# Performance work log

Hardware: AMD Instinct MI355X
Metric: run time of the kernel (lower is better)

## Reference

```python
import jax, jax.numpy as jnp
import numpy as np

N_NODES = 100000
N_EDGES = 3200000
D_FEAT = 256
HIDDEN = 16


def setup_inputs() -> dict:
    key = jax.random.key(0)
    k1, k2, k3, k4 = jax.random.split(key, 4)
    x = jax.random.normal(k1, (N_NODES, D_FEAT), dtype=jnp.float32)
    edge_index = jax.random.randint(k2, (2, N_EDGES), 0, N_NODES, dtype=jnp.int64)
    # GCNConv linear weight (Glorot-ish scale) and bias
    W = jax.random.normal(k3, (D_FEAT, HIDDEN), dtype=jnp.float32) / np.sqrt(D_FEAT)
    b_conv = jnp.zeros((HIDDEN,), dtype=jnp.float32)
    W_fc = jax.random.normal(k4, (HIDDEN, 1), dtype=jnp.float32) / np.sqrt(HIDDEN)
    b_fc = jnp.zeros((1,), dtype=jnp.float32)
    return {"x": x, "edge_index": edge_index, "W": W, "b_conv": b_conv,
            "W_fc": W_fc, "b_fc": b_fc}


def reference(x, edge_index, W, b_conv, W_fc, b_fc):
    N = x.shape[0]
    # --- GCNConv: add self-loops, symmetric normalization, transform, scatter-add ---
    loop = jnp.arange(N, dtype=edge_index.dtype)
    src = jnp.concatenate([edge_index[0], loop])  # message sources (x_j)
    dst = jnp.concatenate([edge_index[1], loop])  # aggregation targets
    # degree of target nodes (edge weights = 1, self-loops included)
    deg = jax.ops.segment_sum(jnp.ones_like(dst, dtype=x.dtype), dst, num_segments=N)
    dinv = jnp.where(deg > 0, jax.lax.rsqrt(deg), 0.0)
    norm = dinv[src] * dinv[dst]  # [E+N]
    h = x @ W                       # [N, hidden] transform before propagation
    msg = h[src] * norm[:, None]    # gather + scale
    agg = jax.ops.segment_sum(msg, dst, num_segments=N)  # scatter-add
    out = agg + b_conv
    return out @ W_fc + b_fc
```

## Files before the change

kernel.cpp:

```cpp
#include <hip/hip_runtime.h>

#define DF 256
#define HID 16
#define WB 512
#define TPB 512
#define PMAX 512

__global__ void sval_kernel(const float* __restrict__ x, const float* __restrict__ Wm,
                            const float* __restrict__ W_fc, float* __restrict__ sv, int N) {
    __shared__ float wl[DF];
    int k = threadIdx.x;
    float a = 0.f;
#pragma unroll
    for (int j = 0; j < HID; ++j) a += Wm[k * HID + j] * W_fc[j];
    wl[k] = a;
    __syncthreads();
    int lane = threadIdx.x & 63;
    int wid = threadIdx.x >> 6;
    float4 wv = reinterpret_cast<const float4*>(wl)[lane];
    for (int row = blockIdx.x * 4 + wid; row < N; row += gridDim.x * 4) {
        float4 xv = reinterpret_cast<const float4*>(x + (size_t)row * DF)[lane];
        float acc = xv.x * wv.x + xv.y * wv.y + xv.z * wv.z + xv.w * wv.w;
#pragma unroll
        for (int off = 32; off > 0; off >>= 1) acc += __shfl_xor(acc, off, 64);
        if (lane == 0) sv[row] = acc;
    }
}

__global__ void sort_kernel(const int* __restrict__ src, const int* __restrict__ dst,
                            unsigned* __restrict__ runStart, unsigned* __restrict__ sorted,
                            int P, int E, int Epw) {
    extern __shared__ unsigned smem[];
    unsigned* pack  = smem;
    unsigned* sortl = pack + Epw;
    unsigned* offs  = sortl + Epw;
    unsigned* cur   = offs + P + 1;
    unsigned short* keyp = (unsigned short*)(cur + P);

    const int w = blockIdx.x;
    const int e0 = w * Epw;
    int m = E - e0; if (m > Epw) m = Epw; if (m < 0) m = 0;

    for (int i = threadIdx.x; i < P; i += blockDim.x) cur[i] = 0;
    __syncthreads();
    for (int i = threadIdx.x; i < m; i += blockDim.x) {
        unsigned s = (unsigned)src[e0 + i];
        unsigned d = (unsigned)dst[e0 + i];
        keyp[i] = (unsigned short)(d >> 8);
        pack[i] = (s << 8) | (d & 255u);
        atomicAdd(&cur[d >> 8], 1u);
    }
    __syncthreads();
    int t = threadIdx.x;
    unsigned v = (t < P) ? cur[t] : 0u;
    sortl[t] = v;
    __syncthreads();
    for (int off = 1; off < blockDim.x; off <<= 1) {
        unsigned u = (t >= off) ? sortl[t - off] : 0u;
        __syncthreads();
        sortl[t] += u;
        __syncthreads();
    }
    if (t < P) offs[t] = sortl[t] - v;
    if (t == 0) offs[P] = (unsigned)m;
    __syncthreads();
    for (int i = threadIdx.x; i < P; i += blockDim.x) cur[i] = offs[i];
    __syncthreads();
    for (int i = threadIdx.x; i < m; i += blockDim.x) {
        unsigned slot = atomicAdd(&cur[keyp[i]], 1u);
        sortl[slot] = pack[i];
    }
    __syncthreads();
    for (int i = threadIdx.x; i < m; i += blockDim.x) sorted[(size_t)e0 + i] = sortl[i];
    for (int p = threadIdx.x; p <= P; p += blockDim.x) runStart[(size_t)p * WB + w] = offs[p];
}

__global__ void degfin_kernel(const unsigned* __restrict__ sorted, const unsigned* __restrict__ runStart,
                              const float* __restrict__ sv, const float* __restrict__ b_conv,
                              const float* __restrict__ W_fc, const float* __restrict__ b_fc,
                              float* __restrict__ dinv, float* __restrict__ tval,
                              float* __restrict__ out, int N, int Epw) {
    __shared__ unsigned dc[256];
    __shared__ float cterm_s;
    const int p = blockIdx.x;
    if (threadIdx.x < 256) dc[threadIdx.x] = 0u;
    if (threadIdx.x == 0) {
        float c = 0.f;
#pragma unroll
        for (int j = 0; j < HID; ++j) c += b_conv[j] * W_fc[j];
        cterm_s = c + b_fc[0];
    }
    __syncthreads();
    const int t = threadIdx.x;
    unsigned s0 = runStart[(size_t)p * WB + t];
    unsigned s1 = runStart[(size_t)(p + 1) * WB + t];
    const unsigned* base = sorted + (size_t)t * Epw;
    for (unsigned j = s0; j < s1; ++j) atomicAdd(&dc[base[j] & 255u], 1u);
    __syncthreads();
    if (threadIdx.x < 256) {
        int i = (p << 8) + threadIdx.x;
        if (i < N) {
            float deg = 1.0f + (float)dc[threadIdx.x];
            float di = rsqrtf(deg);
            float s = sv[i];
            dinv[i] = di;
            tval[i] = s * di;
            out[i] = s / deg + cterm_s;
        }
    }
}

__global__ void reduce_kernel(const unsigned* __restrict__ sorted, const unsigned* __restrict__ runStart,
                              const float* __restrict__ tval, const float* __restrict__ dinv,
                              float* __restrict__ out, int N, int Epw) {
    __shared__ float acc[256];
    const int p = blockIdx.x;
    if (threadIdx.x < 256) acc[threadIdx.x] = 0.f;
    __syncthreads();
    const int t = threadIdx.x;
    unsigned s0 = runStart[(size_t)p * WB + t];
    unsigned s1 = runStart[(size_t)(p + 1) * WB + t];
    const unsigned* base = sorted + (size_t)t * Epw;
    for (unsigned j = s0; j < s1; ++j) {
        unsigned v = base[j];
        atomicAdd(&acc[v & 255u], tval[v >> 8]);
    }
    __syncthreads();
    if (threadIdx.x < 256) {
        int i = (p << 8) + threadIdx.x;
        if (i < N) out[i] += dinv[i] * acc[threadIdx.x];
    }
}

__global__ void fb_count(const int* __restrict__ dst, unsigned* __restrict__ cnt, int E) {
    int stride = gridDim.x * blockDim.x;
    for (int e = blockIdx.x * blockDim.x + threadIdx.x; e < E; e += stride)
        atomicAdd(&cnt[dst[e]], 1u);
}
__global__ void fb_node(const unsigned* __restrict__ cnt, const float* __restrict__ sv,
                        const float* __restrict__ b_conv, const float* __restrict__ W_fc,
                        const float* __restrict__ b_fc, float* __restrict__ dinv,
                        float* __restrict__ tval, float* __restrict__ out, int N) {
    int i = blockIdx.x * blockDim.x + threadIdx.x;
    if (i < N) {
        float c = 0.f;
#pragma unroll
        for (int j = 0; j < HID; ++j) c += b_conv[j] * W_fc[j];
        float deg = 1.0f + (float)cnt[i];
        float di = rsqrtf(deg);
        float s = sv[i];
        dinv[i] = di; tval[i] = s * di;
        out[i] = s / deg + c + b_fc[0];
    }
}
__global__ void fb_scatter(const int* __restrict__ src, const int* __restrict__ dst,
                           const float* __restrict__ tval, const float* __restrict__ dinv,
                           float* __restrict__ out, int E) {
    int stride = gridDim.x * blockDim.x;
    for (int e = blockIdx.x * blockDim.x + threadIdx.x; e < E; e += stride) {
        int si = src[e], di = dst[e];
        atomicAdd(&out[di], tval[si] * dinv[di]);
    }
}

extern "C" void kernel_launch(void* const* d_in, const int* in_sizes, int n_in,
                              void* d_out, int out_size, void* d_ws, size_t ws_size,
                              hipStream_t stream) {
    const float* x      = (const float*)d_in[0];
    const int*   ei     = (const int*)d_in[1];
    const float* Wm     = (const float*)d_in[2];
    const float* b_conv = (const float*)d_in[3];
    const float* W_fc   = (const float*)d_in[4];
    const float* b_fc   = (const float*)d_in[5];
    float* out = (float*)d_out;

    const int N = in_sizes[0] / DF;
    const int E = in_sizes[1] / 2;
    const int* src = ei;
    const int* dst = ei + E;

    const int P   = (N + 255) >> 8;
    const int Epw = (E + WB - 1) / WB;

    char* ws = (char*)d_ws;
    float* sv   = (float*)ws;
    float* dinv = sv + N;
    float* tval = dinv + N;
    unsigned* runStart = (unsigned*)(tval + N);
    unsigned* sorted   = runStart + (size_t)(P + 1) * WB;

    const size_t need = ((size_t)3 * N + (size_t)(P + 1) * WB + (size_t)WB * Epw) * 4;
    const size_t shbytes = (size_t)Epw * 10 + (size_t)(2 * P + 2) * 4 + 64;

    if (P <= PMAX && Epw >= TPB && ws_size >= need && shbytes <= 160 * 1024) {
        sval_kernel<<<2048, 256, 0, stream>>>(x, Wm, W_fc, sv, N);
        sort_kernel<<<WB, TPB, shbytes, stream>>>(src, dst, runStart, sorted, P, E, Epw);
        degfin_kernel<<<P, TPB, 0, stream>>>(sorted, runStart, sv, b_conv, W_fc, b_fc,
                                             dinv, tval, out, N, Epw);
        reduce_kernel<<<P, TPB, 0, stream>>>(sorted, runStart, tval, dinv, out, N, Epw);
    } else {
        unsigned* fcnt = (unsigned*)(tval + N);
        hipMemsetAsync(fcnt, 0, (size_t)N * 4, stream);
        sval_kernel<<<2048, 256, 0, stream>>>(x, Wm, W_fc, sv, N);
        fb_count<<<2048, 256, 0, stream>>>(dst, fcnt, E);
        fb_node<<<(N + 255) / 256, 256, 0, stream>>>(fcnt, sv, b_conv, W_fc, b_fc, dinv, tval, out, N);
        fb_scatter<<<2048, 256, 0, stream>>>(src, dst, tval, dinv, out, E);
    }
}
```

Measured before the change: 97.17 us.

## Fuse sort, degree and reduce stages into one persistent kernel with grid barriers

Merges the sval, sort, degree-finalize and reduce kernels into a single persistent kernel of 512 blocks. Device-wide atomic spin barriers separate the phases, and the sval computation is folded into the sort blocks. This removes three kernel launch gaps and their tail idling, and fuses the self-loop term into the final write so out is no longer read back. It relies on all 512 blocks being co-resident, which is guarded by an occupancy check. It adds a memset launch and barrier spin cost, and the sort's shared-memory footprint limits how many blocks fit per CU.

```diff
diff --git a/kernel.cpp b/kernel.cpp
--- a/kernel.cpp
+++ b/kernel.cpp
@@ -4,7 +4,156 @@
 #define HID 16
 #define WB 512
 #define TPB 512
-#define PMAX 512
+#define NBLK 512
+#define PBITS 8
+#define PMAX 511
+
+__device__ __forceinline__ void gbar(unsigned* cnt, unsigned target) {
+    __syncthreads();
+    if (threadIdx.x == 0) {
+        __hip_atomic_fetch_add(cnt, 1u, __ATOMIC_RELEASE, __HIP_MEMORY_SCOPE_AGENT);
+        unsigned it = 0;
+        while (__hip_atomic_load(cnt, __ATOMIC_ACQUIRE, __HIP_MEMORY_SCOPE_AGENT) < target
+               && ++it < (1u << 24))
+            __builtin_amdgcn_s_sleep(2);
+    }
+    __syncthreads();
+}
+
+extern "C" __global__ void __launch_bounds__(TPB, 4)
+mega_kernel(const float* __restrict__ x, const int* __restrict__ src, const int* __restrict__ dst,
+            const float* __restrict__ Wm, const float* __restrict__ b_conv,
+            const float* __restrict__ W_fc, const float* __restrict__ b_fc,
+            float* __restrict__ sv, float* __restrict__ dinv, float* __restrict__ tval,
+            unsigned* __restrict__ runStart, unsigned* __restrict__ sorted,
+            unsigned* __restrict__ bars, float* __restrict__ out,
+            int N, int E, int P, int Epw) {
+    extern __shared__ unsigned smem[];
+    unsigned* pack  = smem;
+    unsigned* sortl = pack + Epw;
+    unsigned* offs  = sortl + Epw;
+    unsigned* cur   = offs + (P + 1);
+    unsigned short* keyp = (unsigned short*)(cur + P);
+
+    const int w = blockIdx.x;
+    const int e0 = w * Epw;
+    int m = E - e0; if (m > Epw) m = Epw; if (m < 0) m = 0;
+
+    for (int i = threadIdx.x; i < P; i += TPB) cur[i] = 0;
+    __syncthreads();
+    for (int i = threadIdx.x; i < m; i += TPB) {
+        unsigned s = (unsigned)src[e0 + i];
+        unsigned d = (unsigned)dst[e0 + i];
+        keyp[i] = (unsigned short)(d >> PBITS);
+        pack[i] = (s << PBITS) | (d & 255u);
+        atomicAdd(&cur[d >> PBITS], 1u);
+    }
+    __syncthreads();
+    {
+        int t = threadIdx.x;
+        unsigned v = (t < P) ? cur[t] : 0u;
+        sortl[t] = v;
+        __syncthreads();
+        for (int off = 1; off < TPB; off <<= 1) {
+            unsigned u = (t >= off) ? sortl[t - off] : 0u;
+            __syncthreads();
+            sortl[t] += u;
+            __syncthreads();
+        }
+        if (t < P) offs[t] = sortl[t] - v;
+        if (t == 0) offs[P] = (unsigned)m;
+    }
+    __syncthreads();
+    for (int i = threadIdx.x; i < P; i += TPB) cur[i] = offs[i];
+    __syncthreads();
+    for (int i = threadIdx.x; i < m; i += TPB) {
+        unsigned slot = atomicAdd(&cur[keyp[i]], 1u);
+        sortl[slot] = pack[i];
+    }
+    __syncthreads();
+    for (int i = threadIdx.x; i < m; i += TPB) sorted[(size_t)e0 + i] = sortl[i];
+    for (int p = threadIdx.x; p <= P; p += TPB) runStart[(size_t)p * WB + w] = offs[p];
+
+    {
+        int lane = threadIdx.x & 63;
+        int wid  = threadIdx.x >> 6;
+        float a0 = 0.f, a1 = 0.f, a2 = 0.f, a3 = 0.f;
+        const float* wrow = Wm + (size_t)(lane * 4) * HID;
+#pragma unroll
+        for (int j = 0; j < HID; ++j) {
+            float f = W_fc[j];
+            a0 += wrow[j] * f;
+            a1 += wrow[HID + j] * f;
+            a2 += wrow[2 * HID + j] * f;
+            a3 += wrow[3 * HID + j] * f;
+        }
+        for (int row = blockIdx.x * 8 + wid; row < N; row += NBLK * 8) {
+            float4 xv = reinterpret_cast<const float4*>(x + (size_t)row * DF)[lane];
+            float acc = xv.x * a0 + xv.y * a1 + xv.z * a2 + xv.w * a3;
+#pragma unroll
+            for (int off = 32; off > 0; off >>= 1) acc += __shfl_xor(acc, off, 64);
+            if (lane == 0) sv[row] = acc;
+        }
+    }
+
+    gbar(&bars[0], NBLK);
+
+    {
+        unsigned* dc = smem;
+        for (int p = blockIdx.x; p < P; p += NBLK) {
+            if (threadIdx.x < 256) dc[threadIdx.x] = 0u;
+            __syncthreads();
+            unsigned s0 = runStart[(size_t)p * WB + threadIdx.x];
+            unsigned s1 = runStart[(size_t)(p + 1) * WB + threadIdx.x];
+            const unsigned* base = sorted + (size_t)threadIdx.x * Epw;
+            for (unsigned j = s0; j < s1; ++j) atomicAdd(&dc[base[j] & 255u], 1u);
+            __syncthreads();
+            if (threadIdx.x < 256) {
+                int i = (p << PBITS) + threadIdx.x;
+                if (i < N) {
+                    float deg = 1.0f + (float)dc[threadIdx.x];
+                    float di = rsqrtf(deg);
+                    dinv[i] = di;
+                    tval[i] = sv[i] * di;
+                }
+            }
+            __syncthreads();
+        }
+    }
+
+    gbar(&bars[1], NBLK);
+
+    {
+        float* facc = (float*)smem;
+        float cterm;
+        {
+            float c = 0.f;
+#pragma unroll
+            for (int j = 0; j < HID; ++j) c += b_conv[j] * W_fc[j];
+            cterm = c + b_fc[0];
+        }
+        for (int p = blockIdx.x; p < P; p += NBLK) {
+            if (threadIdx.x < 256) facc[threadIdx.x] = 0.f;
+            __syncthreads();
+            unsigned s0 = runStart[(size_t)p * WB + threadIdx.x];
+            unsigned s1 = runStart[(size_t)(p + 1) * WB + threadIdx.x];
+            const unsigned* base = sorted + (size_t)threadIdx.x * Epw;
+            for (unsigned j = s0; j < s1; ++j) {
+                unsigned e = base[j];
+                atomicAdd(&facc[e & 255u], tval[e >> PBITS]);
+            }
+            __syncthreads();
+            if (threadIdx.x < 256) {
+                int i = (p << PBITS) + threadIdx.x;
+                if (i < N) {
+                    float di = dinv[i];
+                    out[i] = sv[i] * di * di + cterm + di * facc[threadIdx.x];
+                }
+            }
+            __syncthreads();
+        }
+    }
+}
 
 __global__ void sval_kernel(const float* __restrict__ x, const float* __restrict__ Wm,
                             const float* __restrict__ W_fc, float* __restrict__ sv, int N) {
@@ -26,112 +175,6 @@
         if (lane == 0) sv[row] = acc;
     }
 }
-
-__global__ void sort_kernel(const int* __restrict__ src, const int* __restrict__ dst,
-                            unsigned* __restrict__ runStart, unsigned* __restrict__ sorted,
-                            int P, int E, int Epw) {
-    extern __shared__ unsigned smem[];
-    unsigned* pack  = smem;
-    unsigned* sortl = pack + Epw;
-    unsigned* offs  = sortl + Epw;
-    unsigned* cur   = offs + P + 1;
-    unsigned short* keyp = (unsigned short*)(cur + P);
-
-    const int w = blockIdx.x;
-    const int e0 = w * Epw;
-    int m = E - e0; if (m > Epw) m = Epw; if (m < 0) m = 0;
-
-    for (int i = threadIdx.x; i < P; i += blockDim.x) cur[i] = 0;
-    __syncthreads();
-    for (int i = threadIdx.x; i < m; i += blockDim.x) {
-        unsigned s = (unsigned)src[e0 + i];
-        unsigned d = (unsigned)dst[e0 + i];
-        keyp[i] = (unsigned short)(d >> 8);
-        pack[i] = (s << 8) | (d & 255u);
-        atomicAdd(&cur[d >> 8], 1u);
-    }
-    __syncthreads();
-    int t = threadIdx.x;
-    unsigned v = (t < P) ? cur[t] : 0u;
-    sortl[t] = v;
-    __syncthreads();
-    for (int off = 1; off < blockDim.x; off <<= 1) {
-        unsigned u = (t >= off) ? sortl[t - off] : 0u;
-        __syncthreads();
-        sortl[t] += u;
-        __syncthreads();
-    }
-    if (t < P) offs[t] = sortl[t] - v;
-    if (t == 0) offs[P] = (unsigned)m;
-    __syncthreads();
-    for (int i = threadIdx.x; i < P; i += blockDim.x) cur[i] = offs[i];
-    __syncthreads();
-    for (int i = threadIdx.x; i < m; i += blockDim.x) {
-        unsigned slot = atomicAdd(&cur[keyp[i]], 1u);
-        sortl[slot] = pack[i];
-    }
-    __syncthreads();
-    for (int i = threadIdx.x; i < m; i += blockDim.x) sorted[(size_t)e0 + i] = sortl[i];
-    for (int p = threadIdx.x; p <= P; p += blockDim.x) runStart[(size_t)p * WB + w] = offs[p];
-}
-
-__global__ void degfin_kernel(const unsigned* __restrict__ sorted, const unsigned* __restrict__ runStart,
-                              const float* __restrict__ sv, const float* __restrict__ b_conv,
-                              const float* __restrict__ W_fc, const float* __restrict__ b_fc,
-                              float* __restrict__ dinv, float* __restrict__ tval,
-                              float* __restrict__ out, int N, int Epw) {
-    __shared__ unsigned dc[256];
-    __shared__ float cterm_s;
-    const int p = blockIdx.x;
-    if (threadIdx.x < 256) dc[threadIdx.x] = 0u;
-    if (threadIdx.x == 0) {
-        float c = 0.f;
-#pragma unroll
-        for (int j = 0; j < HID; ++j) c += b_conv[j] * W_fc[j];
-        cterm_s = c + b_fc[0];
-    }
-    __syncthreads();
-    const int t = threadIdx.x;
-    unsigned s0 = runStart[(size_t)p * WB + t];
-    unsigned s1 = runStart[(size_t)(p + 1) * WB + t];
-    const unsigned* base = sorted + (size_t)t * Epw;
-    for (unsigned j = s0; j < s1; ++j) atomicAdd(&dc[base[j] & 255u], 1u);
-    __syncthreads();
-    if (threadIdx.x < 256) {
-        int i = (p << 8) + threadIdx.x;
-        if (i < N) {
-            float deg = 1.0f + (float)dc[threadIdx.x];
-            float di = rsqrtf(deg);
-            float s = sv[i];
-            dinv[i] = di;
-            tval[i] = s * di;
-            out[i] = s / deg + cterm_s;
-        }
-    }
-}
-
-__global__ void reduce_kernel(const unsigned* __restrict__ sorted, const unsigned* __restrict__ runStart,
-                              const float* __restrict__ tval, const float* __restrict__ dinv,
-                              float* __restrict__ out, int N, int Epw) {
-    __shared__ float acc[256];
-    const int p = blockIdx.x;
-    if (threadIdx.x < 256) acc[threadIdx.x] = 0.f;
-    __syncthreads();
-    const int t = threadIdx.x;
-    unsigned s0 = runStart[(size_t)p * WB + t];
-    unsigned s1 = runStart[(size_t)(p + 1) * WB + t];
-    const unsigned* base = sorted + (size_t)t * Epw;
-    for (unsigned j = s0; j < s1; ++j) {
-        unsigned v = base[j];
-        atomicAdd(&acc[v & 255u], tval[v >> 8]);
-    }
-    __syncthreads();
-    if (threadIdx.x < 256) {
-        int i = (p << 8) + threadIdx.x;
-        if (i < N) out[i] += dinv[i] * acc[threadIdx.x];
-    }
-}
-
 __global__ void fb_count(const int* __restrict__ dst, unsigned* __restrict__ cnt, int E) {
     int stride = gridDim.x * blockDim.x;
     for (int e = blockIdx.x * blockDim.x + threadIdx.x; e < E; e += stride)
@@ -179,25 +222,32 @@
     const int* src = ei;
     const int* dst = ei + E;
 
-    const int P   = (N + 255) >> 8;
+    const int P   = (N + 255) >> PBITS;
     const int Epw = (E + WB - 1) / WB;
 
     char* ws = (char*)d_ws;
-    float* sv   = (float*)ws;
+    unsigned* bars = (unsigned*)ws;
+    float* sv   = (float*)(ws + 64);
     float* dinv = sv + N;
     float* tval = dinv + N;
     unsigned* runStart = (unsigned*)(tval + N);
     unsigned* sorted   = runStart + (size_t)(P + 1) * WB;
 
-    const size_t need = ((size_t)3 * N + (size_t)(P + 1) * WB + (size_t)WB * Epw) * 4;
+    const size_t need = 64 + ((size_t)3 * N + (size_t)(P + 1) * WB + (size_t)WB * Epw) * 4;
     const size_t shbytes = (size_t)Epw * 10 + (size_t)(2 * P + 2) * 4 + 64;
 
-    if (P <= PMAX && Epw >= TPB && ws_size >= need && shbytes <= 160 * 1024) {
-        sval_kernel<<<2048, 256, 0, stream>>>(x, Wm, W_fc, sv, N);
-        sort_kernel<<<WB, TPB, shbytes, stream>>>(src, dst, runStart, sorted, P, E, Epw);
-        degfin_kernel<<<P, TPB, 0, stream>>>(sorted, runStart, sv, b_conv, W_fc, b_fc,
-                                             dinv, tval, out, N, Epw);
-        reduce_kernel<<<P, TPB, 0, stream>>>(sorted, runStart, tval, dinv, out, N, Epw);
+    int maxBlocksPerCU = 0, numCU = 0;
+    bool occ_ok = false;
+    if (hipOccupancyMaxActiveBlocksPerMultiprocessor(&maxBlocksPerCU, mega_kernel, TPB, shbytes)
+            == hipSuccess &&
+        hipDeviceGetAttribute(&numCU, hipDeviceAttributeMultiprocessorCount, 0) == hipSuccess)
+        occ_ok = ((long)maxBlocksPerCU * numCU >= NBLK);
+
+    if (P <= PMAX && Epw >= TPB && ws_size >= need && shbytes <= 160 * 1024 && occ_ok) {
+        hipMemsetAsync(bars, 0, 64, stream);
+        mega_kernel<<<NBLK, TPB, shbytes, stream>>>(x, src, dst, Wm, b_conv, W_fc, b_fc,
+                                                    sv, dinv, tval, runStart, sorted, bars,
+                                                    out, N, E, P, Epw);
     } else {
         unsigned* fcnt = (unsigned*)(tval + N);
         hipMemsetAsync(fcnt, 0, (size_t)N * 4, stream);
```

Result: slower. 309.9 us (+218.9%).

## Double sort blocks, shrink sort LDS, and wave-parallelize bucket reductions

Applied to the files above, without the earlier changes.

The bucket sort now uses 1024 chunks with smaller per-block shared memory. It drops the staged pack/key arrays by reading src/dst twice, and replaces the barrier-heavy Hillis-Steele scan with a wave-shuffle scan. The degree and reduce kernels now assign each 64-lane wave to one chunk's run and stride lanes across it, so loads are coalesced instead of one thread walking each run serially. The self-loop and bias term moves into the reduce kernel so out is written once rather than read-modify-written. The cost is rereading dst from global memory and a larger runStart table.

```diff
diff --git a/kernel.cpp b/kernel.cpp
--- a/kernel.cpp
+++ b/kernel.cpp
@@ -2,8 +2,10 @@
 
 #define DF 256
 #define HID 16
-#define WB 512
-#define TPB 512
+#define WB 1024
+#define STPB 512
+#define WTPB 1024
+#define PBITS 8
 #define PMAX 512
 
 __global__ void sval_kernel(const float* __restrict__ x, const float* __restrict__ Wm,
@@ -31,104 +33,126 @@
                             unsigned* __restrict__ runStart, unsigned* __restrict__ sorted,
                             int P, int E, int Epw) {
     extern __shared__ unsigned smem[];
-    unsigned* pack  = smem;
-    unsigned* sortl = pack + Epw;
-    unsigned* offs  = sortl + Epw;
-    unsigned* cur   = offs + P + 1;
-    unsigned short* keyp = (unsigned short*)(cur + P);
+    unsigned* sortl = smem;
+    unsigned* cur   = sortl + Epw;
+    unsigned* offs  = cur + P;
+    unsigned* wsum  = offs + P + 1;
 
     const int w = blockIdx.x;
-    const int e0 = w * Epw;
-    int m = E - e0; if (m > Epw) m = Epw; if (m < 0) m = 0;
-
-    for (int i = threadIdx.x; i < P; i += blockDim.x) cur[i] = 0;
-    __syncthreads();
-    for (int i = threadIdx.x; i < m; i += blockDim.x) {
+    const size_t e0 = (size_t)w * Epw;
+    int m = (int)((size_t)E > e0 ? (size_t)E - e0 : 0);
+    if (m > Epw) m = Epw;
+
+    for (int i = threadIdx.x; i < P; i += STPB) cur[i] = 0;
+    __syncthreads();
+    for (int i = threadIdx.x; i < m; i += STPB)
+        atomicAdd(&cur[((unsigned)dst[e0 + i]) >> PBITS], 1u);
+    __syncthreads();
+
+    {
+        int t = threadIdx.x, lane = t & 63, wid = t >> 6;
+        unsigned v = (t < P) ? cur[t] : 0u;
+        unsigned xi = v;
+#pragma unroll
+        for (int off = 1; off < 64; off <<= 1) {
+            unsigned u = __shfl_up(xi, off, 64);
+            if (lane >= off) xi += u;
+        }
+        if (lane == 63) wsum[wid] = xi;
+        __syncthreads();
+        if (t < 8) {
+            unsigned u = wsum[t];
+#pragma unroll
+            for (int off = 1; off < 8; off <<= 1) {
+                unsigned uu = __shfl_up(u, off, 64);
+                if (t >= off) u += uu;
+            }
+            wsum[t] = u;
+        }
+        __syncthreads();
+        unsigned excl = xi - v + (wid ? wsum[wid - 1] : 0u);
+        if (t < P) offs[t] = excl;
+        if (t == 0) offs[P] = wsum[7];
+        __syncthreads();
+        for (int i = threadIdx.x; i < P; i += STPB) cur[i] = offs[i];
+    }
+    __syncthreads();
+
+    for (int i = threadIdx.x; i < m; i += STPB) {
         unsigned s = (unsigned)src[e0 + i];
         unsigned d = (unsigned)dst[e0 + i];
-        keyp[i] = (unsigned short)(d >> 8);
-        pack[i] = (s << 8) | (d & 255u);
-        atomicAdd(&cur[d >> 8], 1u);
-    }
-    __syncthreads();
-    int t = threadIdx.x;
-    unsigned v = (t < P) ? cur[t] : 0u;
-    sortl[t] = v;
-    __syncthreads();
-    for (int off = 1; off < blockDim.x; off <<= 1) {
-        unsigned u = (t >= off) ? sortl[t - off] : 0u;
-        __syncthreads();
-        sortl[t] += u;
-        __syncthreads();
-    }
-    if (t < P) offs[t] = sortl[t] - v;
-    if (t == 0) offs[P] = (unsigned)m;
-    __syncthreads();
-    for (int i = threadIdx.x; i < P; i += blockDim.x) cur[i] = offs[i];
-    __syncthreads();
-    for (int i = threadIdx.x; i < m; i += blockDim.x) {
-        unsigned slot = atomicAdd(&cur[keyp[i]], 1u);
-        sortl[slot] = pack[i];
-    }
-    __syncthreads();
-    for (int i = threadIdx.x; i < m; i += blockDim.x) sorted[(size_t)e0 + i] = sortl[i];
-    for (int p = threadIdx.x; p <= P; p += blockDim.x) runStart[(size_t)p * WB + w] = offs[p];
+        unsigned slot = atomicAdd(&cur[d >> PBITS], 1u);
+        sortl[slot] = (s << PBITS) | (d & 255u);
+    }
+    __syncthreads();
+    for (int i = threadIdx.x; i < m; i += STPB) sorted[e0 + i] = sortl[i];
+    for (int pp = threadIdx.x; pp <= P; pp += STPB) runStart[(size_t)pp * WB + w] = offs[pp];
 }
 
 __global__ void degfin_kernel(const unsigned* __restrict__ sorted, const unsigned* __restrict__ runStart,
-                              const float* __restrict__ sv, const float* __restrict__ b_conv,
-                              const float* __restrict__ W_fc, const float* __restrict__ b_fc,
-                              float* __restrict__ dinv, float* __restrict__ tval,
-                              float* __restrict__ out, int N, int Epw) {
+                              const float* __restrict__ sv, float* __restrict__ dinv,
+                              float* __restrict__ tval, int N, int Epw) {
+    __shared__ unsigned s0a[WB], s1a[WB];
     __shared__ unsigned dc[256];
-    __shared__ float cterm_s;
     const int p = blockIdx.x;
+    for (int i = threadIdx.x; i < WB; i += WTPB) {
+        s0a[i] = runStart[(size_t)p * WB + i];
+        s1a[i] = runStart[(size_t)(p + 1) * WB + i];
+    }
     if (threadIdx.x < 256) dc[threadIdx.x] = 0u;
-    if (threadIdx.x == 0) {
-        float c = 0.f;
-#pragma unroll
-        for (int j = 0; j < HID; ++j) c += b_conv[j] * W_fc[j];
-        cterm_s = c + b_fc[0];
-    }
-    __syncthreads();
-    const int t = threadIdx.x;
-    unsigned s0 = runStart[(size_t)p * WB + t];
-    unsigned s1 = runStart[(size_t)(p + 1) * WB + t];
-    const unsigned* base = sorted + (size_t)t * Epw;
-    for (unsigned j = s0; j < s1; ++j) atomicAdd(&dc[base[j] & 255u], 1u);
+    __syncthreads();
+    const int wave = threadIdx.x >> 6, lane = threadIdx.x & 63;
+    for (int w = wave; w < WB; w += (WTPB / 64)) {
+        unsigned s0 = s0a[w], s1 = s1a[w];
+        const unsigned* base = sorted + (size_t)w * Epw;
+        for (unsigned j = s0 + lane; j < s1; j += 64)
+            atomicAdd(&dc[base[j] & 255u], 1u);
+    }
     __syncthreads();
     if (threadIdx.x < 256) {
-        int i = (p << 8) + threadIdx.x;
+        int i = (p << PBITS) + (int)threadIdx.x;
         if (i < N) {
             float deg = 1.0f + (float)dc[threadIdx.x];
             float di = rsqrtf(deg);
-            float s = sv[i];
             dinv[i] = di;
-            tval[i] = s * di;
-            out[i] = s / deg + cterm_s;
+            tval[i] = sv[i] * di;
         }
     }
 }
 
 __global__ void reduce_kernel(const unsigned* __restrict__ sorted, const unsigned* __restrict__ runStart,
                               const float* __restrict__ tval, const float* __restrict__ dinv,
+                              const float* __restrict__ sv, const float* __restrict__ b_conv,
+                              const float* __restrict__ W_fc, const float* __restrict__ b_fc,
                               float* __restrict__ out, int N, int Epw) {
-    __shared__ float acc[256];
+    __shared__ unsigned s0a[WB], s1a[WB];
+    __shared__ float facc[256];
     const int p = blockIdx.x;
-    if (threadIdx.x < 256) acc[threadIdx.x] = 0.f;
-    __syncthreads();
-    const int t = threadIdx.x;
-    unsigned s0 = runStart[(size_t)p * WB + t];
-    unsigned s1 = runStart[(size_t)(p + 1) * WB + t];
-    const unsigned* base = sorted + (size_t)t * Epw;
-    for (unsigned j = s0; j < s1; ++j) {
-        unsigned v = base[j];
-        atomicAdd(&acc[v & 255u], tval[v >> 8]);
+    for (int i = threadIdx.x; i < WB; i += WTPB) {
+        s0a[i] = runStart[(size_t)p * WB + i];
+        s1a[i] = runStart[(size_t)(p + 1) * WB + i];
+    }
+    if (threadIdx.x < 256) facc[threadIdx.x] = 0.f;
+    __syncthreads();
+    const int wave = threadIdx.x >> 6, lane = threadIdx.x & 63;
+    for (int w = wave; w < WB; w += (WTPB / 64)) {
+        unsigned s0 = s0a[w], s1 = s1a[w];
+        const unsigned* base = sorted + (size_t)w * Epw;
+        for (unsigned j = s0 + lane; j < s1; j += 64) {
+            unsigned e = base[j];
+            atomicAdd(&facc[e & 255u], tval[e >> PBITS]);
+        }
     }
     __syncthreads();
     if (threadIdx.x < 256) {
-        int i = (p << 8) + threadIdx.x;
-        if (i < N) out[i] += dinv[i] * acc[threadIdx.x];
+        int i = (p << PBITS) + (int)threadIdx.x;
+        if (i < N) {
+            float c = 0.f;
+#pragma unroll
+            for (int j = 0; j < HID; ++j) c += b_conv[j] * W_fc[j];
+            float di = dinv[i];
+            out[i] = sv[i] * di * di + c + b_fc[0] + di * facc[threadIdx.x];
+        }
     }
 }
 
@@ -179,7 +203,7 @@
     const int* src = ei;
     const int* dst = ei + E;
 
-    const int P   = (N + 255) >> 8;
+    const int P   = (N + 255) >> PBITS;
     const int Epw = (E + WB - 1) / WB;
 
     char* ws = (char*)d_ws;
@@ -190,14 +214,14 @@
     unsigned* sorted   = runStart + (size_t)(P + 1) * WB;
 
     const size_t need = ((size_t)3 * N + (size_t)(P + 1) * WB + (size_t)WB * Epw) * 4;
-    const size_t shbytes = (size_t)Epw * 10 + (size_t)(2 * P + 2) * 4 + 64;
-
-    if (P <= PMAX && Epw >= TPB && ws_size >= need && shbytes <= 160 * 1024) {
+    const size_t shbytes = ((size_t)Epw + 2 * (size_t)P + 9) * 4 + 64;
+
+    if (P >= 1 && P <= PMAX && N <= (1 << 24) && ws_size >= need && shbytes <= 60 * 1024) {
         sval_kernel<<<2048, 256, 0, stream>>>(x, Wm, W_fc, sv, N);
-        sort_kernel<<<WB, TPB, shbytes, stream>>>(src, dst, runStart, sorted, P, E, Epw);
-        degfin_kernel<<<P, TPB, 0, stream>>>(sorted, runStart, sv, b_conv, W_fc, b_fc,
-                                             dinv, tval, out, N, Epw);
-        reduce_kernel<<<P, TPB, 0, stream>>>(sorted, runStart, tval, dinv, out, N, Epw);
+        sort_kernel<<<WB, STPB, shbytes, stream>>>(src, dst, runStart, sorted, P, E, Epw);
+        degfin_kernel<<<P, WTPB, 0, stream>>>(sorted, runStart, sv, dinv, tval, N, Epw);
+        reduce_kernel<<<P, WTPB, 0, stream>>>(sorted, runStart, tval, dinv, sv,
+                                              b_conv, W_fc, b_fc, out, N, Epw);
     } else {
         unsigned* fcnt = (unsigned*)(tval + N);
         hipMemsetAsync(fcnt, 0, (size_t)N * 4, stream);
```

After: 116.1 us. 1.19x slower.
